# Kernel optimization log

Measured on AMD Instinct MI355X. Metric: run time of the kernel, lower is better.

Reference implementation:

```python
import jax, jax.numpy as jnp
import numpy as np

PAD = 1  # padding from init_kwargs

def setup_inputs() -> dict:
    key = jax.random.key(0)
    k1, k2 = jax.random.split(key)
    x = jax.random.normal(k1, (1, 256, 224, 224), dtype=jnp.float32)
    # Conv2d_mvm weight: [out_channels, in_channels, kh, kw]
    weight = jax.random.normal(k2, (256, 256, 3, 3), dtype=jnp.float32) * 0.05
    return {"x": x, "weight": weight}

def reference(x, weight):
    # Exact math of the bit-sliced crossbar conv forward: stride-1 cross-correlation
    # with zero padding, no bias, output squeezed to [C_out, H_out, W_out]
    # (the original forward emits no batch dimension).
    out = jax.lax.conv_general_dilated(
        x, weight,
        window_strides=(1, 1),
        padding=((PAD, PAD), (PAD, PAD)),
        dimension_numbers=("NCHW", "OIHW", "NCHW"),
    )
    return out[0]  # [C_out, H_out, W_out]
```

## Files before the change

kernel.cpp:

```cpp
#include <hip/hip_runtime.h>


#define H 224
#define W 224
#define NPOS (H*W)
#define CI 256
#define CO 256
#define KDIM 2304
#define HP 226
#define XP_ELEMS (HP*HP*CI)
#define AP_ELEMS (CO*KDIM)

typedef __bf16 bf16x8 __attribute__((ext_vector_type(8)));
typedef float f32x4 __attribute__((ext_vector_type(4)));
typedef unsigned short u16x4 __attribute__((ext_vector_type(4)));
typedef unsigned short u16x8 __attribute__((ext_vector_type(8)));

__device__ __forceinline__ unsigned short f2bf(float f) {
    unsigned int u = __float_as_uint(f);
    u += 0x7fff + ((u >> 16) & 1);
    return (unsigned short)(u >> 16);
}

__device__ __forceinline__ void load_lds16(const unsigned short* g, unsigned short* l) {
    __builtin_amdgcn_global_load_lds(
        (const __attribute__((address_space(1))) void*)g,
        (__attribute__((address_space(3))) void*)l,
        16, 0, 0);
}

#define XT_BLOCKS 3136
#define WT_BLOCKS 256
#define BORDER_V8 28800
#define ROW_V8 7232
__global__ void prep_kernel(const float* __restrict__ x, const float* __restrict__ w,
                            unsigned short* __restrict__ ap, unsigned short* __restrict__ xp) {
    __shared__ unsigned short smem[64 * 68];
    const int bx = blockIdx.x;
    const int t = threadIdx.x;

    if (bx < XT_BLOCKS) {
        const unsigned int pBase = (unsigned int)(bx % 784) * 64;
        const unsigned int ciBase = (unsigned int)(bx / 784) * 64;
        {
            const int p4 = (t & 15) * 4;
            const int c0 = t >> 4;
#pragma unroll
            for (int i = 0; i < 4; ++i) {
                const int ci_l = c0 + i * 16;
                const f32x4 v = *(const f32x4*)&x[(ciBase + ci_l) * NPOS + pBase + p4];
                u16x4 s;
                s[0] = f2bf(v[0]); s[1] = f2bf(v[1]); s[2] = f2bf(v[2]); s[3] = f2bf(v[3]);
                *(u16x4*)&smem[ci_l * 68 + p4] = s;
            }
        }
        __syncthreads();
        {
            const int ci0 = (t & 7) * 8;
            const int pr = t >> 3;
#pragma unroll
            for (int j = 0; j < 2; ++j) {
                const int p_l = pr + j * 32;
                const unsigned int p = pBase + p_l;
                const unsigned int hi = p / W, wi = p - hi * W;
                u16x8 v;
#pragma unroll
                for (int k = 0; k < 8; ++k) v[k] = smem[(ci0 + k) * 68 + p_l];
                *(u16x8*)&xp[((hi + 1) * HP + (wi + 1)) * CI + ciBase + ci0] = v;
            }
        }
    } else if (bx < XT_BLOCKS + WT_BLOCKS) {
        const int co = bx - XT_BLOCKS;
        const float* wc = w + co * KDIM;
#pragma unroll
        for (int i = 0; i < 9; ++i)
            smem[i * 256 + t] = f2bf(wc[i * 256 + t]);
        __syncthreads();
        unsigned short* apc = ap + co * KDIM;
#pragma unroll
        for (int tap = 0; tap < 9; ++tap)
            apc[tap * 256 + t] = smem[t * 9 + tap];
    } else {
        const int idx = (bx - XT_BLOCKS - WT_BLOCKS) * 256 + t;
        if (idx < BORDER_V8) {
            unsigned short* p;
            if (idx < 2 * ROW_V8) {
                const int r = idx / ROW_V8;
                const int off = idx - r * ROW_V8;
                p = xp + r * (225 * HP * CI) + off * 8;
            } else {
                const int i2 = idx - 2 * ROW_V8;
                const int seg = i2 >> 5;
                const int o = i2 & 31;
                const int hp = 1 + (seg >> 1);
                const int wp = (seg & 1) * 225;
                p = xp + (hp * HP + wp) * CI + o * 8;
            }
            *(u16x8*)p = (u16x8){0, 0, 0, 0, 0, 0, 0, 0};
        }
    }
}


#define READ_A(base, half)                                                      \
    _Pragma("unroll")                                                           \
    for (int mi = 0; mi < 4; ++mi)                                              \
        af[mi] = *(const bf16x8*)&lds[(base) + arow + ((half) * 4 + mi) * 512];

#define READ_B(base)                                                            \
    _Pragma("unroll")                                                           \
    for (int ni = 0; ni < 4; ++ni)                                              \
        bf[ni] = *(const bf16x8*)&lds[(base) + brow + ni * 512];

#define MFMA16(half)                                                            \
    __builtin_amdgcn_s_setprio(1);                                              \
    _Pragma("unroll")                                                           \
    for (int mi = 0; mi < 4; ++mi)                                              \
        _Pragma("unroll")                                                       \
        for (int ni = 0; ni < 4; ++ni)                                          \
            acc[(half) * 4 + mi][ni] = __builtin_amdgcn_mfma_f32_16x16x32_bf16( \
                af[mi], bf[ni], acc[(half) * 4 + mi][ni], 0, 0, 0);             \
    __builtin_amdgcn_s_setprio(0);

__global__ __launch_bounds__(512, 1) void gemm_conv_kernel(
    const unsigned short* __restrict__ Ap,
    const unsigned short* __restrict__ Xp,
    float* __restrict__ out)
{
    __shared__ unsigned short lds[65536];

    const int tid = threadIdx.x;
    const int Nb = blockIdx.x;
    const int wave = tid >> 6;
    const int wm = wave >> 2;
    const int wn = wave & 3;
    const int lane = tid & 63;
    const int ln15 = lane & 15;
    const int quad = lane >> 4;
    const int slot8 = (quad ^ ((ln15 >> 1) & 3)) * 8;
    const int arow = (wm * 128 + ln15) * 32 + slot8;
    const int brow = 32768 + (wn * 64 + ln15) * 32 + slot8;

    const int c4 = (tid & 3) ^ ((tid >> 3) & 3);
    const unsigned short* a_src[2];
    const unsigned short* b_src[2];
#pragma unroll
    for (int j = 0; j < 2; ++j) {
        const int r = j * 128 + (tid >> 2);
        a_src[j] = Ap + r * KDIM + c4 * 8;
        unsigned int p = Nb * 256 + r;
        unsigned int hi = p / W, wi = p - hi * W;
        b_src[j] = Xp + (hi * HP + wi) * CI + c4 * 8;
    }

    f32x4 acc[8][4];
#pragma unroll
    for (int mi = 0; mi < 8; ++mi)
#pragma unroll
        for (int ni = 0; ni < 4; ++ni)
            acc[mi][ni] = (f32x4){0.f, 0.f, 0.f, 0.f};

    auto stageA = [&](int kt, int k) {
        const int dst = ((kt & 1) * 2 + k) * 8192;
        const int off = kt * 64 + k * 32;
#pragma unroll
        for (int j = 0; j < 2; ++j)
            load_lds16(a_src[j] + off, &lds[dst + (j * 8 + wave) * 512]);
    };
    auto stageB = [&](int kt, int k) {
        const int dst = 32768 + ((kt & 1) * 2 + k) * 8192;
        const int tap = kt >> 2;
        const int dh = (tap * 11) >> 5;
        const int dw = tap - dh * 3;
        const int off = (dh * HP + dw) * CI + (kt & 3) * 64 + k * 32;
#pragma unroll
        for (int j = 0; j < 2; ++j)
            load_lds16(b_src[j] + off, &lds[dst + (j * 8 + wave) * 512]);
    };

    bf16x8 af[4], bf[4];

    stageA(0, 0); stageB(0, 0); stageA(0, 1); stageB(0, 1);
    asm volatile("s_waitcnt vmcnt(4)" ::: "memory");
    __builtin_amdgcn_s_barrier();

    for (int kt = 0; kt < 36; ++kt) {
        const int pi = (kt & 1) * 2;
        const int b0 = pi * 8192;
        const int b1 = (pi + 1) * 8192;
        const bool st = kt < 35;
        READ_A(b0, 0) READ_B(b0)
        if (st) stageA(kt + 1, 0);
        MFMA16(0)
        READ_A(b0, 1)
        if (st) stageB(kt + 1, 0);
        MFMA16(1)
        if (st) asm volatile("s_waitcnt vmcnt(4)" ::: "memory");
        else    asm volatile("s_waitcnt vmcnt(0)" ::: "memory");
        __builtin_amdgcn_s_barrier();
        READ_A(b1, 0) READ_B(b1)
        if (st) stageA(kt + 1, 1);
        MFMA16(0)
        READ_A(b1, 1)
        if (st) stageB(kt + 1, 1);
        MFMA16(1)
        if (st) {
            asm volatile("s_waitcnt vmcnt(4)" ::: "memory");
            __builtin_amdgcn_s_barrier();
        }
    }

    const int pcol = Nb * 256 + wn * 64 + ln15;
    const int corow = wm * 128 + quad * 4;
#pragma unroll
    for (int mi = 0; mi < 8; ++mi)
#pragma unroll
        for (int ni = 0; ni < 4; ++ni)
#pragma unroll
            for (int r = 0; r < 4; ++r)
                out[(corow + mi * 16 + r) * NPOS + pcol + ni * 16] = acc[mi][ni][r];
}

extern "C" void kernel_launch(void* const* d_in, const int* in_sizes, int n_in,
                              void* d_out, int out_size, void* d_ws, size_t ws_size,
                              hipStream_t stream) {
    const float* x = (const float*)d_in[0];
    const float* w = (const float*)d_in[1];
    float* out = (float*)d_out;

    unsigned short* xp = (unsigned short*)d_ws;
    unsigned short* ap = xp + XP_ELEMS;

    prep_kernel<<<XT_BLOCKS + WT_BLOCKS + 113, 256, 0, stream>>>(x, w, ap, xp);
    gemm_conv_kernel<<<dim3(NPOS / 256), 512, 0, stream>>>(ap, xp, out);
}
```

Before: 154.0 us.

## Issue all next-tile global loads upfront and read full LDS fragments before MFMAs

Restructures the GEMM main loop so that all eight global-to-LDS loads for the next K tile are issued at the start of each iteration, rather than interleaved between MFMA halves. All A and B fragments for a 32-wide K slice are read from LDS in one batch into separate register arrays, followed by 32 back-to-back MFMAs. The wait counts are adjusted to match (vmcnt 8, then 4). This gives memory latency more time to hide and removes LDS-read stalls in the middle of the MFMA sequence, at the cost of extra VGPRs for the second A fragment set.

New measurement: 165.5 us. +7.5%, slower.

```diff
diff --git a/kernel.cpp b/kernel.cpp
--- a/kernel.cpp
+++ b/kernel.cpp
@@ -102,24 +102,25 @@
 }
 
 
-#define READ_A(base, half)                                                      \
+#define RDALL(base)                                                             \
     _Pragma("unroll")                                                           \
     for (int mi = 0; mi < 4; ++mi)                                              \
-        af[mi] = *(const bf16x8*)&lds[(base) + arow + ((half) * 4 + mi) * 512];
-
-#define READ_B(base)                                                            \
+        afA[mi] = *(const bf16x8*)&lds[(base) + arow + mi * 512];               \
+    _Pragma("unroll")                                                           \
+    for (int mi = 0; mi < 4; ++mi)                                              \
+        afB[mi] = *(const bf16x8*)&lds[(base) + arow + (4 + mi) * 512];         \
     _Pragma("unroll")                                                           \
     for (int ni = 0; ni < 4; ++ni)                                              \
-        bf[ni] = *(const bf16x8*)&lds[(base) + brow + ni * 512];
-
-#define MFMA16(half)                                                            \
+        bfr[ni] = *(const bf16x8*)&lds[(base) + brow + ni * 512];
+
+#define MMH(half, afX)                                                          \
     __builtin_amdgcn_s_setprio(1);                                              \
     _Pragma("unroll")                                                           \
     for (int mi = 0; mi < 4; ++mi)                                              \
         _Pragma("unroll")                                                       \
         for (int ni = 0; ni < 4; ++ni)                                          \
             acc[(half) * 4 + mi][ni] = __builtin_amdgcn_mfma_f32_16x16x32_bf16( \
-                af[mi], bf[ni], acc[(half) * 4 + mi][ni], 0, 0, 0);             \
+                afX[mi], bfr[ni], acc[(half) * 4 + mi][ni], 0, 0, 0);           \
     __builtin_amdgcn_s_setprio(0);
 
 __global__ __launch_bounds__(512, 1) void gemm_conv_kernel(
@@ -177,33 +178,31 @@
         for (int j = 0; j < 2; ++j)
             load_lds16(b_src[j] + off, &lds[dst + (j * 8 + wave) * 512]);
     };
-
-    bf16x8 af[4], bf[4];
-
-    stageA(0, 0); stageB(0, 0); stageA(0, 1); stageB(0, 1);
+    auto stage8 = [&](int kt) {
+        stageA(kt, 0); stageB(kt, 0);
+        stageA(kt, 1); stageB(kt, 1);
+    };
+
+    bf16x8 afA[4], afB[4], bfr[4];
+
+    stage8(0);
     asm volatile("s_waitcnt vmcnt(4)" ::: "memory");
     __builtin_amdgcn_s_barrier();
 
     for (int kt = 0; kt < 36; ++kt) {
-        const int pi = (kt & 1) * 2;
-        const int b0 = pi * 8192;
-        const int b1 = (pi + 1) * 8192;
+        const int b0 = (kt & 1) * 16384;
+        const int b1 = b0 + 8192;
         const bool st = kt < 35;
-        READ_A(b0, 0) READ_B(b0)
-        if (st) stageA(kt + 1, 0);
-        MFMA16(0)
-        READ_A(b0, 1)
-        if (st) stageB(kt + 1, 0);
-        MFMA16(1)
-        if (st) asm volatile("s_waitcnt vmcnt(4)" ::: "memory");
+        if (st) stage8(kt + 1);
+        RDALL(b0)
+        MMH(0, afA)
+        MMH(1, afB)
+        if (st) asm volatile("s_waitcnt vmcnt(8)" ::: "memory");
         else    asm volatile("s_waitcnt vmcnt(0)" ::: "memory");
         __builtin_amdgcn_s_barrier();
-        READ_A(b1, 0) READ_B(b1)
-        if (st) stageA(kt + 1, 1);
-        MFMA16(0)
-        READ_A(b1, 1)
-        if (st) stageB(kt + 1, 1);
-        MFMA16(1)
+        RDALL(b1)
+        MMH(0, afA)
+        MMH(1, afB)
         if (st) {
             asm volatile("s_waitcnt vmcnt(4)" ::: "memory");
             __builtin_amdgcn_s_barrier();
```

## Shrink GEMM N-tile to one image row and regrid waves as 4x2

Applied to the files above, without the earlier changes.

The pixel tile per block goes from 256 to 224 (one output row), so the grid grows from 196 to 224 blocks. The aim is to balance the 256 CUs of MI355X better and cut tail waste. Waves are rearranged into a 4x2 layout, each computing 64 output channels by 112 pixels with 4x7 MFMA tiles. The LDS fragment reads are reordered to match. Staging still loads 256 B-rows per tile, so 32 rows are fetched and never used, and the per-wave tile shape is less square, which costs a little LDS read efficiency.

Measured after the change: 153.2 us, median of 2. About the same (-0.5%).

```diff
diff --git a/kernel.cpp b/kernel.cpp
--- a/kernel.cpp
+++ b/kernel.cpp
@@ -10,6 +10,7 @@
 #define HP 226
 #define XP_ELEMS (HP*HP*CI)
 #define AP_ELEMS (CO*KDIM)
+#define BN 224
 
 typedef __bf16 bf16x8 __attribute__((ext_vector_type(8)));
 typedef float f32x4 __attribute__((ext_vector_type(4)));
@@ -102,24 +103,15 @@
 }
 
 
-#define READ_A(base, half)                                                      \
-    _Pragma("unroll")                                                           \
-    for (int mi = 0; mi < 4; ++mi)                                              \
-        af[mi] = *(const bf16x8*)&lds[(base) + arow + ((half) * 4 + mi) * 512];
-
-#define READ_B(base)                                                            \
-    _Pragma("unroll")                                                           \
-    for (int ni = 0; ni < 4; ++ni)                                              \
-        bf[ni] = *(const bf16x8*)&lds[(base) + brow + ni * 512];
-
-#define MFMA16(half)                                                            \
+#define MFMA14(miA, miB)                                                        \
     __builtin_amdgcn_s_setprio(1);                                              \
     _Pragma("unroll")                                                           \
-    for (int mi = 0; mi < 4; ++mi)                                              \
-        _Pragma("unroll")                                                       \
-        for (int ni = 0; ni < 4; ++ni)                                          \
-            acc[(half) * 4 + mi][ni] = __builtin_amdgcn_mfma_f32_16x16x32_bf16( \
-                af[mi], bf[ni], acc[(half) * 4 + mi][ni], 0, 0, 0);             \
+    for (int ni = 0; ni < 7; ++ni) {                                            \
+        acc[miA][ni] = __builtin_amdgcn_mfma_f32_16x16x32_bf16(                 \
+            af[miA], bf[ni], acc[miA][ni], 0, 0, 0);                            \
+        acc[miB][ni] = __builtin_amdgcn_mfma_f32_16x16x32_bf16(                 \
+            af[miB], bf[ni], acc[miB][ni], 0, 0, 0);                            \
+    }                                                                           \
     __builtin_amdgcn_s_setprio(0);
 
 __global__ __launch_bounds__(512, 1) void gemm_conv_kernel(
@@ -132,14 +124,14 @@
     const int tid = threadIdx.x;
     const int Nb = blockIdx.x;
     const int wave = tid >> 6;
-    const int wm = wave >> 2;
-    const int wn = wave & 3;
+    const int wm = wave >> 1;
+    const int wn = wave & 1;
     const int lane = tid & 63;
     const int ln15 = lane & 15;
     const int quad = lane >> 4;
     const int slot8 = (quad ^ ((ln15 >> 1) & 3)) * 8;
-    const int arow = (wm * 128 + ln15) * 32 + slot8;
-    const int brow = 32768 + (wn * 64 + ln15) * 32 + slot8;
+    const int arow = (wm * 64 + ln15) * 32 + slot8;
+    const int brow = 32768 + (wn * 112 + ln15) * 32 + slot8;
 
     const int c4 = (tid & 3) ^ ((tid >> 3) & 3);
     const unsigned short* a_src[2];
@@ -148,16 +140,16 @@
     for (int j = 0; j < 2; ++j) {
         const int r = j * 128 + (tid >> 2);
         a_src[j] = Ap + r * KDIM + c4 * 8;
-        unsigned int p = Nb * 256 + r;
+        unsigned int p = Nb * BN + r;
         unsigned int hi = p / W, wi = p - hi * W;
         b_src[j] = Xp + (hi * HP + wi) * CI + c4 * 8;
     }
 
-    f32x4 acc[8][4];
-#pragma unroll
-    for (int mi = 0; mi < 8; ++mi)
-#pragma unroll
-        for (int ni = 0; ni < 4; ++ni)
+    f32x4 acc[4][7];
+#pragma unroll
+    for (int mi = 0; mi < 4; ++mi)
+#pragma unroll
+        for (int ni = 0; ni < 7; ++ni)
             acc[mi][ni] = (f32x4){0.f, 0.f, 0.f, 0.f};
 
     auto stageA = [&](int kt, int k) {
@@ -178,44 +170,56 @@
             load_lds16(b_src[j] + off, &lds[dst + (j * 8 + wave) * 512]);
     };
 
-    bf16x8 af[4], bf[4];
+    bf16x8 af[4], bf[7];
+
+#define RD_MAIN(base)                                                           \
+    _Pragma("unroll")                                                           \
+    for (int mi = 0; mi < 2; ++mi)                                              \
+        af[mi] = *(const bf16x8*)&lds[(base) + arow + mi * 512];                \
+    _Pragma("unroll")                                                           \
+    for (int ni = 0; ni < 7; ++ni)                                              \
+        bf[ni] = *(const bf16x8*)&lds[(base) + brow + ni * 512];
+
+#define RD_TAILA(base)                                                          \
+    _Pragma("unroll")                                                           \
+    for (int mi = 2; mi < 4; ++mi)                                              \
+        af[mi] = *(const bf16x8*)&lds[(base) + arow + mi * 512];
 
     stageA(0, 0); stageB(0, 0); stageA(0, 1); stageB(0, 1);
     asm volatile("s_waitcnt vmcnt(4)" ::: "memory");
     __builtin_amdgcn_s_barrier();
 
     for (int kt = 0; kt < 36; ++kt) {
-        const int pi = (kt & 1) * 2;
-        const int b0 = pi * 8192;
-        const int b1 = (pi + 1) * 8192;
+        const int b0 = (kt & 1) * 16384;
+        const int b1 = b0 + 8192;
         const bool st = kt < 35;
-        READ_A(b0, 0) READ_B(b0)
+        RD_MAIN(b0)
         if (st) stageA(kt + 1, 0);
-        MFMA16(0)
-        READ_A(b0, 1)
+        MFMA14(0, 1)
+        RD_TAILA(b0)
         if (st) stageB(kt + 1, 0);
-        MFMA16(1)
+        MFMA14(2, 3)
         if (st) asm volatile("s_waitcnt vmcnt(4)" ::: "memory");
         else    asm volatile("s_waitcnt vmcnt(0)" ::: "memory");
         __builtin_amdgcn_s_barrier();
-        READ_A(b1, 0) READ_B(b1)
+        RD_MAIN(b1)
         if (st) stageA(kt + 1, 1);
-        MFMA16(0)
-        READ_A(b1, 1)
+        MFMA14(0, 1)
+        RD_TAILA(b1)
         if (st) stageB(kt + 1, 1);
-        MFMA16(1)
+        MFMA14(2, 3)
         if (st) {
             asm volatile("s_waitcnt vmcnt(4)" ::: "memory");
             __builtin_amdgcn_s_barrier();
         }
     }
 
-    const int pcol = Nb * 256 + wn * 64 + ln15;
-    const int corow = wm * 128 + quad * 4;
-#pragma unroll
-    for (int mi = 0; mi < 8; ++mi)
-#pragma unroll
-        for (int ni = 0; ni < 4; ++ni)
+    const int pcol = Nb * BN + wn * 112 + ln15;
+    const int corow = wm * 64 + quad * 4;
+#pragma unroll
+    for (int mi = 0; mi < 4; ++mi)
+#pragma unroll
+        for (int ni = 0; ni < 7; ++ni)
 #pragma unroll
             for (int r = 0; r < 4; ++r)
                 out[(corow + mi * 16 + r) * NPOS + pcol + ni * 16] = acc[mi][ni][r];
@@ -232,5 +236,5 @@
     unsigned short* ap = xp + XP_ELEMS;
 
     prep_kernel<<<XT_BLOCKS + WT_BLOCKS + 113, 256, 0, stream>>>(x, w, ap, xp);
-    gemm_conv_kernel<<<dim3(NPOS / 256), 512, 0, stream>>>(ap, xp, out);
-}
+    gemm_conv_kernel<<<dim3(NPOS / BN), 512, 0, stream>>>(ap, xp, out);
+}
```
